# Performance work log

Measured on AMD Instinct MI355X. Metric: run time of the kernel, lower is better.

Reference implementation:

```python
import jax, jax.numpy as jnp
import numpy as np

B, S, D, H, DH, DF = 8, 1024, 512, 8, 64, 2048
EPS = 1e-5


def layer_norm(x, g, b):
    mu = jnp.mean(x, axis=-1, keepdims=True)
    var = jnp.mean(jnp.square(x - mu), axis=-1, keepdims=True)
    return (x - mu) * jax.lax.rsqrt(var + EPS) * g + b


def rel_shift(x):
    # Transformer-XL relative shift: [b,h,q,k] -> shifted [b,h,q,k]
    b, h, q, k = x.shape
    x = jnp.pad(x, ((0, 0), (0, 0), (0, 0), (1, 0)))
    x = x.reshape(b, h, k + 1, q)[:, :, 1:, :].reshape(b, h, q, k)
    return x


def setup_inputs() -> dict:
    key = jax.random.key(0)
    ks = jax.random.split(key, 16)
    sc = 0.02
    inp = {
        'x': jax.random.normal(ks[0], (B, S, D), jnp.float32),
        'rel_positions': jax.random.normal(ks[1], (S, D), jnp.float32),
        'mask': jnp.triu(jnp.ones((S, S), jnp.bool_), k=1),  # True = masked (causal)
        'Wq': jax.random.normal(ks[2], (D, D), jnp.float32) * sc,
        'Wk': jax.random.normal(ks[3], (D, D), jnp.float32) * sc,
        'Wv': jax.random.normal(ks[4], (D, D), jnp.float32) * sc,
        'Wr': jax.random.normal(ks[5], (D, D), jnp.float32) * sc,
        'Wo': jax.random.normal(ks[6], (D, D), jnp.float32) * sc,
        'u_bias': jax.random.normal(ks[7], (H, DH), jnp.float32) * sc,
        'v_bias': jax.random.normal(ks[8], (H, DH), jnp.float32) * sc,
        'ln1_g': jnp.ones((D,), jnp.float32),
        'ln1_b': jnp.zeros((D,), jnp.float32),
        'W1': jax.random.normal(ks[9], (D, DF), jnp.float32) * sc,
        'b1': jnp.zeros((DF,), jnp.float32),
        'W2': jax.random.normal(ks[10], (DF, D), jnp.float32) * sc,
        'b2': jnp.zeros((D,), jnp.float32),
        'ln2_g': jnp.ones((D,), jnp.float32),
        'ln2_b': jnp.zeros((D,), jnp.float32),
    }
    return inp


def reference(x, rel_positions, mask, Wq, Wk, Wv, Wr, Wo, u_bias, v_bias,
              ln1_g, ln1_b, W1, b1, W2, b2, ln2_g, ln2_b):
    b, s, d = x.shape
    q = (x @ Wq).reshape(b, s, H, DH)
    k = (x @ Wk).reshape(b, s, H, DH)
    v = (x @ Wv).reshape(b, s, H, DH)
    r = (rel_positions @ Wr).reshape(s, H, DH)
    # content term (q + u) k^T and position term (q + v) r^T with rel-shift
    ac = jnp.einsum('bqhd,bkhd->bhqk', q + u_bias, k)
    bd = rel_shift(jnp.einsum('bqhd,khd->bhqk', q + v_bias, r))
    scores = (ac + bd) * (1.0 / np.sqrt(DH))
    scores = jnp.where(mask[None, None, :, :], jnp.asarray(-1e9, scores.dtype), scores)
    attn = jax.nn.softmax(scores, axis=-1)
    ctx = jnp.einsum('bhqk,bkhd->bqhd', attn, v).reshape(b, s, d) @ Wo
    h1 = layer_norm(x + ctx, ln1_g, ln1_b)
    ff = jax.nn.relu(h1 @ W1 + b1) @ W2 + b2
    out = layer_norm(h1 + ff, ln2_g, ln2_b)
    return out, attn
```

## Files before the change

### kernel.cpp

```cpp
#include <hip/hip_runtime.h>
#include <hip/hip_bf16.h>

typedef __hip_bfloat16 bf16;

#define NB 8
#define NS 1024
#define ND 512
#define NH 8
#define NDH 64
#define NDF 2048

typedef __attribute__((ext_vector_type(8))) short s16x8;
typedef __attribute__((ext_vector_type(4))) float f32x4;

__device__ __forceinline__ void storev(float* p, float v) { *p = v; }
__device__ __forceinline__ void storev(bf16* p, float v) { *p = __float2bfloat16(v); }
__device__ __forceinline__ short f2bf(float f) {
    bf16 h = __float2bfloat16(f);
    return *reinterpret_cast<short*>(&h);
}
__device__ __forceinline__ float bf2f(short s) {
    bf16 h = *reinterpret_cast<bf16*>(&s);
    return __bfloat162float(h);
}

__device__ __forceinline__ void gload_lds16(const short* g, short* l) {
    __builtin_amdgcn_global_load_lds(
        (const __attribute__((address_space(1))) unsigned int*)g,
        (__attribute__((address_space(3))) unsigned int*)l, 16, 0, 0);
}

__global__ __launch_bounds__(256) void cast2_kernel(
    const float4* __restrict__ inA, int n4a,
    const float4* __restrict__ inB, int n4b,
    short* __restrict__ outA, short* __restrict__ outB)
{
    int i = blockIdx.x * 256 + threadIdx.x;
    const float4* s; short* d; int j;
    if (i < n4a) { s = inA; d = outA; j = i; }
    else if (i < n4a + n4b) { s = inB; d = outB; j = i - n4a; }
    else return;
    float4 v = s[j];
    short4 o;
    o.x = f2bf(v.x); o.y = f2bf(v.y); o.z = f2bf(v.z); o.w = f2bf(v.w);
    *reinterpret_cast<short4*>(d + (size_t)j * 4) = o;
}

struct TP7 {
    const float* src[7];
    short* dst[7];
    int K[7];
    int N[7];
};

__global__ __launch_bounds__(256) void transpose_cast_all_kernel(TP7 p)
{
    __shared__ float t[32][33];
    const int z = blockIdx.z;
    const float* src = p.src[z];
    short* dst = p.dst[z];
    const int K = p.K[z], N = p.N[z];
    const int ntx = N >> 5;
    const int f = blockIdx.x;
    if (f >= ntx * (K >> 5)) return;
    const int n0 = (f % ntx) * 32, k0 = (f / ntx) * 32;
    const int tx = threadIdx.x & 31, ty = threadIdx.x >> 5;
#pragma unroll
    for (int i = 0; i < 4; ++i)
        t[ty + i * 8][tx] = src[(size_t)(k0 + ty + i * 8) * N + n0 + tx];
    __syncthreads();
#pragma unroll
    for (int i = 0; i < 4; ++i)
        dst[(size_t)(n0 + ty + i * 8) * K + k0 + tx] = f2bf(t[tx][ty + i * 8]);
}

__global__ __launch_bounds__(256) void transpose_v_kernel(
    const short* __restrict__ v, short* __restrict__ vT)
{
    __shared__ short t[32][33];
    const int s0 = blockIdx.x * 32, n0 = blockIdx.y * 32;
    const int bh = blockIdx.z;
    const int h = bh & (NH - 1), b = bh >> 3;
    const int tx = threadIdx.x & 31, ty = threadIdx.x >> 5;
#pragma unroll
    for (int i = 0; i < 4; ++i)
        t[ty + i * 8][tx] = v[(size_t)(b * NS + s0 + ty + i * 8) * ND + h * NDH + n0 + tx];
    __syncthreads();
#pragma unroll
    for (int i = 0; i < 4; ++i)
        vT[((size_t)bh * NDH + n0 + ty + i * 8) * NS + s0 + tx] = t[tx][ty + i * 8];
}

template <typename CT>
__global__ __launch_bounds__(256) void mfma_gemm_kernel(
    const short* __restrict__ A, const short* __restrict__ Bt,
    const float* __restrict__ bias, CT* __restrict__ C,
    int M, int N, int K, int doRelu)
{
    __shared__ __align__(16) short As[128 * 32];
    __shared__ __align__(16) short Bs[128 * 32];
    const int row0 = blockIdx.y * 128;
    const int col0 = blockIdx.x * 128;
    const int tid = threadIdx.x;
    const int lane = tid & 63, w = tid >> 6;
    const int wm = w >> 1, wn = w & 1;
    const int lm = lane & 15, kq = lane >> 4;
    const int srow = lane >> 2;
    const int schk = lane & 3;

    f32x4 acc[4][4] = {};

    for (int k0 = 0; k0 < K; k0 += 32) {
#pragma unroll
        for (int p = 0; p < 2; ++p) {
            int rbase = p * 64 + w * 16;
            int r = rbase + srow;
            int gc = schk ^ ((r >> 1) & 3);
            gload_lds16(A  + (size_t)(row0 + r) * K + k0 + gc * 8, As + rbase * 32);
            gload_lds16(Bt + (size_t)(col0 + r) * K + k0 + gc * 8, Bs + rbase * 32);
        }
        __syncthreads();

        s16x8 af[4], bfr[4];
#pragma unroll
        for (int i = 0; i < 4; ++i) {
            int ra = wm * 64 + i * 16 + lm;
            int rb = wn * 64 + i * 16 + lm;
            af[i]  = *reinterpret_cast<const s16x8*>(As + ra * 32 + (kq ^ ((ra >> 1) & 3)) * 8);
            bfr[i] = *reinterpret_cast<const s16x8*>(Bs + rb * 32 + (kq ^ ((rb >> 1) & 3)) * 8);
        }
#pragma unroll
        for (int i = 0; i < 4; ++i)
#pragma unroll
            for (int j = 0; j < 4; ++j)
                acc[i][j] = __builtin_amdgcn_mfma_f32_16x16x32_bf16(
                    af[i], bfr[j], acc[i][j], 0, 0, 0);
        __syncthreads();
    }

#pragma unroll
    for (int i = 0; i < 4; ++i) {
        int cr0 = row0 + wm * 64 + i * 16 + kq * 4;
#pragma unroll
        for (int j = 0; j < 4; ++j) {
            int cc = col0 + wn * 64 + j * 16 + lm;
            float bv = bias ? bias[cc] : 0.0f;
#pragma unroll
            for (int r = 0; r < 4; ++r) {
                float v = acc[i][j][r] + bv;
                if (doRelu) v = fmaxf(v, 0.0f);
                storev(&C[(size_t)(cr0 + r) * N + cc], v);
            }
        }
    }
}

template <typename CT>
__global__ __launch_bounds__(256) void mfma_gemm64_kernel(
    const short* __restrict__ A, const short* __restrict__ Bt,
    const float* __restrict__ bias, CT* __restrict__ C,
    int M, int N, int K, int doRelu)
{
    __shared__ __align__(16) short As[128 * 32];
    __shared__ __align__(16) short Bs[64 * 32];
    const int row0 = blockIdx.y * 128;
    const int col0 = blockIdx.x * 64;
    const int tid = threadIdx.x;
    const int lane = tid & 63, w = tid >> 6;
    const int wm = w >> 1, wn = w & 1;
    const int lm = lane & 15, kq = lane >> 4;
    const int srow = lane >> 2;
    const int schk = lane & 3;

    f32x4 acc[4][2] = {};

    for (int k0 = 0; k0 < K; k0 += 32) {
#pragma unroll
        for (int p = 0; p < 2; ++p) {
            int rbase = p * 64 + w * 16;
            int r = rbase + srow;
            int gc = schk ^ ((r >> 1) & 3);
            gload_lds16(A + (size_t)(row0 + r) * K + k0 + gc * 8, As + rbase * 32);
        }
        {
            int rbase = w * 16;
            int r = rbase + srow;
            int gc = schk ^ ((r >> 1) & 3);
            gload_lds16(Bt + (size_t)(col0 + r) * K + k0 + gc * 8, Bs + rbase * 32);
        }
        __syncthreads();

        s16x8 af[4], bfr[2];
#pragma unroll
        for (int i = 0; i < 4; ++i) {
            int ra = wm * 64 + i * 16 + lm;
            af[i] = *reinterpret_cast<const s16x8*>(As + ra * 32 + (kq ^ ((ra >> 1) & 3)) * 8);
        }
#pragma unroll
        for (int j = 0; j < 2; ++j) {
            int rb = wn * 32 + j * 16 + lm;
            bfr[j] = *reinterpret_cast<const s16x8*>(Bs + rb * 32 + (kq ^ ((rb >> 1) & 3)) * 8);
        }
#pragma unroll
        for (int i = 0; i < 4; ++i)
#pragma unroll
            for (int j = 0; j < 2; ++j)
                acc[i][j] = __builtin_amdgcn_mfma_f32_16x16x32_bf16(
                    af[i], bfr[j], acc[i][j], 0, 0, 0);
        __syncthreads();
    }

#pragma unroll
    for (int i = 0; i < 4; ++i) {
        int cr0 = row0 + wm * 64 + i * 16 + kq * 4;
#pragma unroll
        for (int j = 0; j < 2; ++j) {
            int cc = col0 + wn * 32 + j * 16 + lm;
            float bv = bias ? bias[cc] : 0.0f;
#pragma unroll
            for (int r = 0; r < 4; ++r) {
                float v = acc[i][j][r] + bv;
                if (doRelu) v = fmaxf(v, 0.0f);
                storev(&C[(size_t)(cr0 + r) * N + cc], v);
            }
        }
    }
}

__global__ __launch_bounds__(256) void qkv_gemm_kernel(
    const short* __restrict__ A, const short* __restrict__ Bt,
    const float* __restrict__ ub, const float* __restrict__ vb,
    short* __restrict__ qu, short* __restrict__ qv,
    short* __restrict__ kb, short* __restrict__ vbuf, int K)
{
    __shared__ __align__(16) short As[128 * 32];
    __shared__ __align__(16) short Bs[128 * 32];
    const int row0 = blockIdx.y * 128;
    const int col0 = blockIdx.x * 128;
    const int tid = threadIdx.x;
    const int lane = tid & 63, w = tid >> 6;
    const int wm = w >> 1, wn = w & 1;
    const int lm = lane & 15, kq = lane >> 4;
    const int srow = lane >> 2;
    const int schk = lane & 3;

    f32x4 acc[4][4] = {};

    for (int k0 = 0; k0 < K; k0 += 32) {
#pragma unroll
        for (int p = 0; p < 2; ++p) {
            int rbase = p * 64 + w * 16;
            int r = rbase + srow;
            int gc = schk ^ ((r >> 1) & 3);
            gload_lds16(A  + (size_t)(row0 + r) * K + k0 + gc * 8, As + rbase * 32);
            gload_lds16(Bt + (size_t)(col0 + r) * K + k0 + gc * 8, Bs + rbase * 32);
        }
        __syncthreads();

        s16x8 af[4], bfr[4];
#pragma unroll
        for (int i = 0; i < 4; ++i) {
            int ra = wm * 64 + i * 16 + lm;
            int rb = wn * 64 + i * 16 + lm;
            af[i]  = *reinterpret_cast<const s16x8*>(As + ra * 32 + (kq ^ ((ra >> 1) & 3)) * 8);
            bfr[i] = *reinterpret_cast<const s16x8*>(Bs + rb * 32 + (kq ^ ((rb >> 1) & 3)) * 8);
        }
#pragma unroll
        for (int i = 0; i < 4; ++i)
#pragma unroll
            for (int j = 0; j < 4; ++j)
                acc[i][j] = __builtin_amdgcn_mfma_f32_16x16x32_bf16(
                    af[i], bfr[j], acc[i][j], 0, 0, 0);
        __syncthreads();
    }

    const int sec = col0 >> 9;
#pragma unroll
    for (int i = 0; i < 4; ++i) {
        int cr0 = row0 + wm * 64 + i * 16 + kq * 4;
#pragma unroll
        for (int j = 0; j < 4; ++j) {
            int cc = col0 + wn * 64 + j * 16 + lm;
            int c5 = cc & 511;
#pragma unroll
            for (int r = 0; r < 4; ++r) {
                float a = acc[i][j][r];
                size_t idx = (size_t)(cr0 + r) * ND + c5;
                if (sec == 0) {
                    qu[idx] = f2bf(a + ub[c5]);
                    qv[idx] = f2bf(a + vb[c5]);
                } else if (sec == 1) {
                    kb[idx] = f2bf(a);
                } else {
                    vbuf[idx] = f2bf(a);
                }
            }
        }
    }
}

__global__ __launch_bounds__(256) void fused_attn_kernel(
    const short* __restrict__ qu, const short* __restrict__ qv,
    const short* __restrict__ kb, const short* __restrict__ rb,
    const short* __restrict__ vT, float* __restrict__ attn,
    short* __restrict__ ctx)
{
    __shared__ __align__(16) short K_s[64][72];
    __shared__ __align__(16) short V_s[64][72];
    __shared__ __align__(16) short r_s[128][72];
    __shared__ __align__(16) short bd_s[64][80];

    const int bid = blockIdx.x;
    const int strip = 15 - (bid >> 6);
    const int bh = bid & 63;
    const int h = bh & (NH - 1), b = bh >> 3;
    const int q0 = strip * 64;
    const int n_kt = strip + 1;
    const int tid = threadIdx.x;
    const int lane = tid & 63, w = tid >> 6;
    const int lm = lane & 15, kq = lane >> 4;
    const int woff = 48 - w * 16;

    s16x8 aq[2], av[2];
#pragma unroll
    for (int ks = 0; ks < 2; ++ks) {
        const size_t off = (size_t)(b * NS + q0 + w * 16 + lm) * ND + h * NDH + ks * 32 + kq * 8;
        aq[ks] = *reinterpret_cast<const s16x8*>(qu + off);
        av[ks] = *reinterpret_cast<const s16x8*>(qv + off);
    }

    f32x4 apv[4] = {};
    float linv[4];

    for (int pass = 0; pass < 2; ++pass) {
        float lsum[4] = {0.f, 0.f, 0.f, 0.f};
        for (int kt = 0; kt < n_kt; ++kt) {
            const int k0 = kt * 64;
            const int u_base = k0 - q0 + 960;
            __syncthreads();
#pragma unroll
            for (int l = 0; l < 2; ++l) {
                int idx = tid + l * 256;
                int r = idx >> 3, c = idx & 7;
                *reinterpret_cast<s16x8*>(&K_s[r][c * 8]) =
                    *reinterpret_cast<const s16x8*>(kb + (size_t)(b * NS + k0 + r) * ND + h * NDH + c * 8);
            }
            if (pass) {
#pragma unroll
                for (int l = 0; l < 2; ++l) {
                    int idx = tid + l * 256;
                    int r = idx >> 3, c = idx & 7;
                    *reinterpret_cast<s16x8*>(&V_s[r][c * 8]) =
                        *reinterpret_cast<const s16x8*>(vT + ((size_t)bh * NDH + r) * NS + k0 + c * 8);
                }
            }
#pragma unroll
            for (int l = 0; l < 4; ++l) {
                int idx = tid + l * 256;
                int rr = idx >> 3, c = idx & 7;
                int ur = u_base + rr; ur = ur > 1023 ? 1023 : ur;
                *reinterpret_cast<s16x8*>(&r_s[rr][c * 8]) =
                    *reinterpret_cast<const s16x8*>(rb + (size_t)ur * ND + h * NDH + c * 8);
            }
            __syncthreads();

            f32x4 aac[4] = {};
            f32x4 abd[5] = {};
#pragma unroll
            for (int ks = 0; ks < 2; ++ks) {
#pragma unroll
                for (int j = 0; j < 4; ++j) {
                    s16x8 bk = *reinterpret_cast<const s16x8*>(&K_s[j * 16 + lm][ks * 32 + kq * 8]);
                    aac[j] = __builtin_amdgcn_mfma_f32_16x16x32_bf16(aq[ks], bk, aac[j], 0, 0, 0);
                }
#pragma unroll
                for (int j = 0; j < 5; ++j) {
                    s16x8 br = *reinterpret_cast<const s16x8*>(&r_s[woff + j * 16 + lm][ks * 32 + kq * 8]);
                    abd[j] = __builtin_amdgcn_mfma_f32_16x16x32_bf16(av[ks], br, abd[j], 0, 0, 0);
                }
            }
#pragma unroll
            for (int j = 0; j < 5; ++j)
#pragma unroll
                for (int r = 0; r < 4; ++r)
                    bd_s[w * 16 + kq * 4 + r][j * 16 + lm] = f2bf(abd[j][r]);

            float sv[4][4];
#pragma unroll
            for (int jj = 0; jj < 4; ++jj)
#pragma unroll
                for (int r = 0; r < 4; ++r) {
                    int c = jj * 16 + lm - kq * 4 - r + 15;
                    sv[jj][r] = (aac[jj][r] + bf2f(bd_s[w * 16 + kq * 4 + r][c])) * 0.125f;
                }

            if (pass == 0) {
#pragma unroll
                for (int jj = 0; jj < 4; ++jj)
#pragma unroll
                    for (int r = 0; r < 4; ++r) {
                        int q_ls = w * 16 + kq * 4 + r;
                        bool ok = (k0 + jj * 16 + lm) <= (q0 + q_ls);
                        lsum[r] += ok ? __expf(sv[jj][r]) : 0.0f;
                    }
            } else {
                short* ew = &bd_s[w * 16][0];
#pragma unroll
                for (int jj = 0; jj < 4; ++jj)
#pragma unroll
                    for (int r = 0; r < 4; ++r) {
                        int q_ls = w * 16 + kq * 4 + r;
                        int kk = k0 + jj * 16 + lm;
                        bool ok = kk <= (q0 + q_ls);
                        float a = ok ? __expf(sv[jj][r]) * linv[r] : 0.0f;
                        attn[((size_t)bh * NS + q0 + q_ls) * NS + kk] = a;
                        ew[(kq * 4 + r) * 80 + jj * 16 + lm] = f2bf(a);
                    }
#pragma unroll
                for (int ks = 0; ks < 2; ++ks) {
                    s16x8 ae = *reinterpret_cast<const s16x8*>(ew + lm * 80 + ks * 32 + kq * 8);
#pragma unroll
                    for (int jn = 0; jn < 4; ++jn) {
                        s16x8 bv = *reinterpret_cast<const s16x8*>(&V_s[jn * 16 + lm][ks * 32 + kq * 8]);
                        apv[jn] = __builtin_amdgcn_mfma_f32_16x16x32_bf16(ae, bv, apv[jn], 0, 0, 0);
                    }
                }
            }
        }
        if (pass == 0) {
#pragma unroll
            for (int r = 0; r < 4; ++r) {
                float v = lsum[r];
                v += __shfl_xor(v, 1); v += __shfl_xor(v, 2);
                v += __shfl_xor(v, 4); v += __shfl_xor(v, 8);
                linv[r] = 1.0f / v;
            }
        }
    }

    const int z = NS - n_kt * 64;
    if (z > 0) {
        const int z4 = z >> 2;
        float4 zz = make_float4(0.f, 0.f, 0.f, 0.f);
        for (int i = tid; i < 64 * z4; i += 256) {
            int zr = i / z4, zc = i - zr * z4;
            *reinterpret_cast<float4*>(
                attn + ((size_t)bh * NS + q0 + zr) * NS + n_kt * 64 + zc * 4) = zz;
        }
    }
#pragma unroll
    for (int jn = 0; jn < 4; ++jn)
#pragma unroll
        for (int r = 0; r < 4; ++r)
            ctx[(size_t)(b * NS + q0 + w * 16 + kq * 4 + r) * ND + h * NDH + jn * 16 + lm] =
                f2bf(apv[jn][r]);
}

__global__ __launch_bounds__(256) void add_ln_kernel(
    const float* __restrict__ xin, const float* __restrict__ yin,
    const float* __restrict__ g, const float* __restrict__ bb,
    float* __restrict__ out, short* __restrict__ out_bf)
{
    __shared__ float red[4];
    __shared__ float red2[4];
    const int row = blockIdx.x;
    const size_t base = (size_t)row * ND;
    const int tid = threadIdx.x;
    const int lane = tid & 63, w = tid >> 6;

    float v0 = xin[base + tid] + yin[base + tid];
    float v1 = xin[base + tid + 256] + yin[base + tid + 256];
    float s = v0 + v1;
#pragma unroll
    for (int o = 32; o > 0; o >>= 1) s += __shfl_xor(s, o);
    if (lane == 0) red[w] = s;
    __syncthreads();
    float mu = (red[0] + red[1] + red[2] + red[3]) * (1.0f / ND);
    float d0 = v0 - mu, d1 = v1 - mu;
    float vs = d0 * d0 + d1 * d1;
#pragma unroll
    for (int o = 32; o > 0; o >>= 1) vs += __shfl_xor(vs, o);
    if (lane == 0) red2[w] = vs;
    __syncthreads();
    float var = (red2[0] + red2[1] + red2[2] + red2[3]) * (1.0f / ND);
    float rs = rsqrtf(var + 1e-5f);
    float o0 = d0 * rs * g[tid] + bb[tid];
    float o1 = d1 * rs * g[tid + 256] + bb[tid + 256];
    out[base + tid] = o0;
    out[base + tid + 256] = o1;
    if (out_bf) {
        out_bf[base + tid] = f2bf(o0);
        out_bf[base + tid + 256] = f2bf(o1);
    }
}

extern "C" void kernel_launch(void* const* d_in, const int* in_sizes, int n_in,
                              void* d_out, int out_size, void* d_ws, size_t ws_size,
                              hipStream_t stream)
{
    const float* x   = (const float*)d_in[0];
    const float* rel = (const float*)d_in[1];
    const float* Wq = (const float*)d_in[3];
    const float* Wk = (const float*)d_in[4];
    const float* Wv = (const float*)d_in[5];
    const float* Wr = (const float*)d_in[6];
    const float* Wo = (const float*)d_in[7];
    const float* ub = (const float*)d_in[8];
    const float* vb = (const float*)d_in[9];
    const float* g1 = (const float*)d_in[10];
    const float* be1 = (const float*)d_in[11];
    const float* W1 = (const float*)d_in[12];
    const float* bb1 = (const float*)d_in[13];
    const float* W2 = (const float*)d_in[14];
    const float* bb2 = (const float*)d_in[15];
    const float* g2 = (const float*)d_in[16];
    const float* be2 = (const float*)d_in[17];

    float* out0 = (float*)d_out;
    float* attn = out0 + (size_t)NB * NS * ND;

    char* ws = (char*)d_ws;
    const size_t SZ_F32 = (size_t)NB * NS * ND * 4;
    const size_t SZ_BF  = (size_t)NB * NS * ND * 2;
    const size_t SZ_MID = (size_t)NB * NS * NDF * 2;
    const size_t SZ_RBF = (size_t)NS * ND * 2;
    const size_t SZ_W   = (size_t)ND * ND * 2;
    const size_t SZ_W12 = (size_t)ND * NDF * 2;
    const size_t needed = 2 * SZ_F32 + 8 * SZ_BF + SZ_MID + 2 * SZ_RBF + 5 * SZ_W + 2 * SZ_W12;
    if (ws_size < needed) return;

    float* tmp  = (float*)ws; ws += SZ_F32;
    float* h1   = (float*)ws; ws += SZ_F32;
    short* x_bf = (short*)ws; ws += SZ_BF;
    short* qu_bf = (short*)ws; ws += SZ_BF;
    short* qv_bf = (short*)ws; ws += SZ_BF;
    short* k_bf = (short*)ws; ws += SZ_BF;
    short* vbuf = (short*)ws; ws += SZ_BF;
    short* vT   = (short*)ws; ws += SZ_BF;
    short* ctx  = (short*)ws; ws += SZ_BF;
    short* h1b  = (short*)ws; ws += SZ_BF;
    short* mid  = (short*)ws; ws += SZ_MID;
    short* rel_bf = (short*)ws; ws += SZ_RBF;
    short* r_bf   = (short*)ws; ws += SZ_RBF;
    short* Wqkv = (short*)ws; ws += 3 * SZ_W;
    short* WrT = (short*)ws; ws += SZ_W;
    short* WoT = (short*)ws; ws += SZ_W;
    short* W1T = (short*)ws; ws += SZ_W12;
    short* W2T = (short*)ws; ws += SZ_W12;

    dim3 blk(256);
    const int M = NB * NS;

    cast2_kernel<<<dim3((M * ND / 4 + NS * ND / 4 + 255) / 256), blk, 0, stream>>>(
        (const float4*)x, M * ND / 4, (const float4*)rel, NS * ND / 4, x_bf, rel_bf);
    TP7 tp;
    tp.src[0] = Wq; tp.dst[0] = Wqkv;                 tp.K[0] = ND;  tp.N[0] = ND;
    tp.src[1] = Wk; tp.dst[1] = Wqkv + (size_t)ND * ND;     tp.K[1] = ND;  tp.N[1] = ND;
    tp.src[2] = Wv; tp.dst[2] = Wqkv + (size_t)2 * ND * ND; tp.K[2] = ND;  tp.N[2] = ND;
    tp.src[3] = Wr; tp.dst[3] = WrT;                  tp.K[3] = ND;  tp.N[3] = ND;
    tp.src[4] = Wo; tp.dst[4] = WoT;                  tp.K[4] = ND;  tp.N[4] = ND;
    tp.src[5] = W1; tp.dst[5] = W1T;                  tp.K[5] = ND;  tp.N[5] = NDF;
    tp.src[6] = W2; tp.dst[6] = W2T;                  tp.K[6] = NDF; tp.N[6] = ND;
    transpose_cast_all_kernel<<<dim3(1024, 1, 7), blk, 0, stream>>>(tp);

    qkv_gemm_kernel<<<dim3(3 * ND / 128, M / 128), blk, 0, stream>>>(
        x_bf, Wqkv, ub, vb, qu_bf, qv_bf, k_bf, vbuf, ND);
    mfma_gemm64_kernel<bf16><<<dim3(ND / 64, NS / 128), blk, 0, stream>>>(
        rel_bf, WrT, nullptr, (bf16*)r_bf, NS, ND, ND, 0);
    transpose_v_kernel<<<dim3(NS / 32, NDH / 32, NB * NH), blk, 0, stream>>>(vbuf, vT);

    fused_attn_kernel<<<dim3(NB * NH * 16), blk, 0, stream>>>(
        qu_bf, qv_bf, k_bf, r_bf, vT, attn, ctx);

    mfma_gemm64_kernel<float><<<dim3(ND / 64, M / 128), blk, 0, stream>>>(
        ctx, WoT, nullptr, tmp, M, ND, ND, 0);
    add_ln_kernel<<<dim3(M), blk, 0, stream>>>(x, tmp, g1, be1, h1, h1b);

    mfma_gemm_kernel<bf16><<<dim3(NDF / 128, M / 128), blk, 0, stream>>>(
        h1b, W1T, bb1, (bf16*)mid, M, NDF, ND, 1);
    mfma_gemm64_kernel<float><<<dim3(ND / 64, M / 128), blk, 0, stream>>>(
        mid, W2T, bb2, tmp, M, ND, NDF, 0);
    add_ln_kernel<<<dim3(M), blk, 0, stream>>>(h1, tmp, g2, be2, out0, nullptr);
}
```

Before: 307.1 us.

## Merge rel projection into QKV GEMM and reuse rel tiles with async swizzled LDS loads

Folds the rel_positions @ Wr projection into the QKV GEMM launch as extra column blocks, which removes one kernel launch. In the attention kernel, K/V/r tiles are now loaded with direct global-to-LDS loads into XOR-swizzled unpadded buffers. The 128-row r window is kept as a two-slot ring, so each key tile fetches only 64 new rows. MFMA sections are raised in wave priority. The merged grid wastes some blocks that exit early, and the ring indexing adds complexity.

```diff
diff --git a/kernel.cpp b/kernel.cpp
--- a/kernel.cpp
+++ b/kernel.cpp
@@ -227,16 +227,23 @@
     }
 }
 
-__global__ __launch_bounds__(256) void qkv_gemm_kernel(
-    const short* __restrict__ A, const short* __restrict__ Bt,
+__global__ __launch_bounds__(256) void qkvr_gemm_kernel(
+    const short* __restrict__ x_bf, const short* __restrict__ Wqkv,
+    const short* __restrict__ rel_bf, const short* __restrict__ WrT,
     const float* __restrict__ ub, const float* __restrict__ vb,
     short* __restrict__ qu, short* __restrict__ qv,
-    short* __restrict__ kb, short* __restrict__ vbuf, int K)
-{
+    short* __restrict__ kb, short* __restrict__ vbuf,
+    short* __restrict__ r_bf)
+{
+    const int isRel = blockIdx.x >= 12;
+    if (isRel && blockIdx.y >= 8) return;
+    const short* A  = isRel ? rel_bf : x_bf;
+    const short* Bt = isRel ? WrT : Wqkv;
+    const int col0 = isRel ? (blockIdx.x - 12) * 128 : blockIdx.x * 128;
+    const int row0 = blockIdx.y * 128;
+
     __shared__ __align__(16) short As[128 * 32];
     __shared__ __align__(16) short Bs[128 * 32];
-    const int row0 = blockIdx.y * 128;
-    const int col0 = blockIdx.x * 128;
     const int tid = threadIdx.x;
     const int lane = tid & 63, w = tid >> 6;
     const int wm = w >> 1, wn = w & 1;
@@ -246,14 +253,14 @@
 
     f32x4 acc[4][4] = {};
 
-    for (int k0 = 0; k0 < K; k0 += 32) {
+    for (int k0 = 0; k0 < ND; k0 += 32) {
 #pragma unroll
         for (int p = 0; p < 2; ++p) {
             int rbase = p * 64 + w * 16;
             int r = rbase + srow;
             int gc = schk ^ ((r >> 1) & 3);
-            gload_lds16(A  + (size_t)(row0 + r) * K + k0 + gc * 8, As + rbase * 32);
-            gload_lds16(Bt + (size_t)(col0 + r) * K + k0 + gc * 8, Bs + rbase * 32);
+            gload_lds16(A  + (size_t)(row0 + r) * ND + k0 + gc * 8, As + rbase * 32);
+            gload_lds16(Bt + (size_t)(col0 + r) * ND + k0 + gc * 8, Bs + rbase * 32);
         }
         __syncthreads();
 
@@ -286,7 +293,9 @@
             for (int r = 0; r < 4; ++r) {
                 float a = acc[i][j][r];
                 size_t idx = (size_t)(cr0 + r) * ND + c5;
-                if (sec == 0) {
+                if (isRel) {
+                    r_bf[idx] = f2bf(a);
+                } else if (sec == 0) {
                     qu[idx] = f2bf(a + ub[c5]);
                     qv[idx] = f2bf(a + vb[c5]);
                 } else if (sec == 1) {
@@ -305,9 +314,9 @@
     const short* __restrict__ vT, float* __restrict__ attn,
     short* __restrict__ ctx)
 {
-    __shared__ __align__(16) short K_s[64][72];
-    __shared__ __align__(16) short V_s[64][72];
-    __shared__ __align__(16) short r_s[128][72];
+    __shared__ __align__(16) short K_s[64 * 64];
+    __shared__ __align__(16) short V_s[64 * 64];
+    __shared__ __align__(16) short r_s[2][64 * 64];
     __shared__ __align__(16) short bd_s[64][80];
 
     const int bid = blockIdx.x;
@@ -320,6 +329,8 @@
     const int lane = tid & 63, w = tid >> 6;
     const int lm = lane & 15, kq = lane >> 4;
     const int woff = 48 - w * 16;
+    const int srow8 = lane >> 3;
+    const int schk8 = lane & 7;
 
     s16x8 aq[2], av[2];
 #pragma unroll
@@ -336,49 +347,73 @@
         float lsum[4] = {0.f, 0.f, 0.f, 0.f};
         for (int kt = 0; kt < n_kt; ++kt) {
             const int k0 = kt * 64;
-            const int u_base = k0 - q0 + 960;
+            const int ub0 = k0 - q0 + 960;
             __syncthreads();
 #pragma unroll
-            for (int l = 0; l < 2; ++l) {
-                int idx = tid + l * 256;
-                int r = idx >> 3, c = idx & 7;
-                *reinterpret_cast<s16x8*>(&K_s[r][c * 8]) =
-                    *reinterpret_cast<const s16x8*>(kb + (size_t)(b * NS + k0 + r) * ND + h * NDH + c * 8);
+            for (int p = 0; p < 2; ++p) {
+                int rbase = p * 32 + w * 8;
+                int grow = rbase + srow8;
+                int gc = schk8 ^ (grow & 7);
+                gload_lds16(kb + (size_t)(b * NS + k0 + grow) * ND + h * NDH + gc * 8,
+                            K_s + rbase * 64);
             }
             if (pass) {
 #pragma unroll
-                for (int l = 0; l < 2; ++l) {
-                    int idx = tid + l * 256;
-                    int r = idx >> 3, c = idx & 7;
-                    *reinterpret_cast<s16x8*>(&V_s[r][c * 8]) =
-                        *reinterpret_cast<const s16x8*>(vT + ((size_t)bh * NDH + r) * NS + k0 + c * 8);
+                for (int p = 0; p < 2; ++p) {
+                    int rbase = p * 32 + w * 8;
+                    int grow = rbase + srow8;
+                    int gc = schk8 ^ (grow & 7);
+                    gload_lds16(vT + ((size_t)bh * NDH + grow) * NS + k0 + gc * 8,
+                                V_s + rbase * 64);
                 }
             }
-#pragma unroll
-            for (int l = 0; l < 4; ++l) {
-                int idx = tid + l * 256;
-                int rr = idx >> 3, c = idx & 7;
-                int ur = u_base + rr; ur = ur > 1023 ? 1023 : ur;
-                *reinterpret_cast<s16x8*>(&r_s[rr][c * 8]) =
-                    *reinterpret_cast<const s16x8*>(rb + (size_t)ur * ND + h * NDH + c * 8);
+            if (kt == 0) {
+#pragma unroll
+                for (int half = 0; half < 2; ++half)
+#pragma unroll
+                    for (int p = 0; p < 2; ++p) {
+                        int rbase = p * 32 + w * 8;
+                        int grow = rbase + srow8;
+                        int ur = ub0 + half * 64 + grow; ur = ur > 1023 ? 1023 : ur;
+                        int gc = schk8 ^ (grow & 7);
+                        gload_lds16(rb + (size_t)ur * ND + h * NDH + gc * 8,
+                                    r_s[half] + rbase * 64);
+                    }
+            } else {
+#pragma unroll
+                for (int p = 0; p < 2; ++p) {
+                    int rbase = p * 32 + w * 8;
+                    int grow = rbase + srow8;
+                    int ur = ub0 + 64 + grow; ur = ur > 1023 ? 1023 : ur;
+                    int gc = schk8 ^ (grow & 7);
+                    gload_lds16(rb + (size_t)ur * ND + h * NDH + gc * 8,
+                                r_s[(kt + 1) & 1] + rbase * 64);
+                }
             }
             __syncthreads();
 
             f32x4 aac[4] = {};
             f32x4 abd[5] = {};
+            __builtin_amdgcn_s_setprio(1);
 #pragma unroll
             for (int ks = 0; ks < 2; ++ks) {
 #pragma unroll
                 for (int j = 0; j < 4; ++j) {
-                    s16x8 bk = *reinterpret_cast<const s16x8*>(&K_s[j * 16 + lm][ks * 32 + kq * 8]);
+                    int rr = j * 16 + lm;
+                    s16x8 bk = *reinterpret_cast<const s16x8*>(
+                        K_s + rr * 64 + ((4 * ks + kq) ^ (lm & 7)) * 8);
                     aac[j] = __builtin_amdgcn_mfma_f32_16x16x32_bf16(aq[ks], bk, aac[j], 0, 0, 0);
                 }
 #pragma unroll
                 for (int j = 0; j < 5; ++j) {
-                    s16x8 br = *reinterpret_cast<const s16x8*>(&r_s[woff + j * 16 + lm][ks * 32 + kq * 8]);
+                    int rr = woff + j * 16 + lm;
+                    const short* rbuf = r_s[(kt + (rr >> 6)) & 1];
+                    s16x8 br = *reinterpret_cast<const s16x8*>(
+                        rbuf + (rr & 63) * 64 + ((4 * ks + kq) ^ (lm & 7)) * 8);
                     abd[j] = __builtin_amdgcn_mfma_f32_16x16x32_bf16(av[ks], br, abd[j], 0, 0, 0);
                 }
             }
+            __builtin_amdgcn_s_setprio(0);
 #pragma unroll
             for (int j = 0; j < 5; ++j)
 #pragma unroll
@@ -421,7 +456,8 @@
                     s16x8 ae = *reinterpret_cast<const s16x8*>(ew + lm * 80 + ks * 32 + kq * 8);
 #pragma unroll
                     for (int jn = 0; jn < 4; ++jn) {
-                        s16x8 bv = *reinterpret_cast<const s16x8*>(&V_s[jn * 16 + lm][ks * 32 + kq * 8]);
+                        s16x8 bv = *reinterpret_cast<const s16x8*>(
+                            V_s + (jn * 16 + lm) * 64 + ((4 * ks + kq) ^ (lm & 7)) * 8);
                         apv[jn] = __builtin_amdgcn_mfma_f32_16x16x32_bf16(ae, bv, apv[jn], 0, 0, 0);
                     }
                 }
@@ -563,10 +599,8 @@
     tp.src[6] = W2; tp.dst[6] = W2T;                  tp.K[6] = NDF; tp.N[6] = ND;
     transpose_cast_all_kernel<<<dim3(1024, 1, 7), blk, 0, stream>>>(tp);
 
-    qkv_gemm_kernel<<<dim3(3 * ND / 128, M / 128), blk, 0, stream>>>(
-        x_bf, Wqkv, ub, vb, qu_bf, qv_bf, k_bf, vbuf, ND);
-    mfma_gemm64_kernel<bf16><<<dim3(ND / 64, NS / 128), blk, 0, stream>>>(
-        rel_bf, WrT, nullptr, (bf16*)r_bf, NS, ND, ND, 0);
+    qkvr_gemm_kernel<<<dim3(16, M / 128), blk, 0, stream>>>(
+        x_bf, Wqkv, rel_bf, WrT, ub, vb, qu_bf, qv_bf, k_bf, vbuf, r_bf);
     transpose_v_kernel<<<dim3(NS / 32, NDH / 32, NB * NH), blk, 0, stream>>>(vbuf, vT);
 
     fused_attn_kernel<<<dim3(NB * NH * 16), blk, 0, stream>>>(
```

Result: faster. 299.5 us (-2.4%).
